# Kernel tuning notes

Hardware: AMD Instinct MI355X
Metric: run time of the kernel (lower is better)

Reference implementation:

```python
import jax, jax.numpy as jnp
import numpy as np

DATA_DIM = 2048
COORD_DIM = 2
NUM_V = DATA_DIM // COORD_DIM  # 1024 vertices
HID = 256
TDIM = 128
NUM_LAYERS = 4
B = 512


def _sinusoidal(t, dim=TDIM):
    half = dim // 2
    freqs = jnp.exp(-jnp.log(10000.0) * jnp.arange(half, dtype=jnp.float32) / (half - 1))
    ang = t.astype(jnp.float32)[:, None] * freqs[None, :]  # (B, half)
    return jnp.concatenate([jnp.sin(ang), jnp.cos(ang)], axis=1)  # (B, dim)


def _cycle_agg(h):
    # degree-3 cycle graph (self + next + prev), values 1/3 each == circular-shift mean
    # h: (B, V, D)
    return (h + jnp.roll(h, -1, axis=1) + jnp.roll(h, 1, axis=1)) * (1.0 / 3.0)


def setup_inputs() -> dict:
    key = jax.random.key(0)
    ks = jax.random.split(key, 16)
    dims = [COORD_DIM + TDIM] + [HID] * NUM_LAYERS  # [130,256,256,256,256]

    def glorot(k, shape):
        fan_in = shape[0]
        return jax.random.normal(k, shape, dtype=jnp.float32) / jnp.sqrt(jnp.float32(fan_in))

    inp = {
        'x': jax.random.normal(ks[0], (B, DATA_DIM), dtype=jnp.float32),
        't': jax.random.randint(ks[1], (B,), 0, 1000, dtype=jnp.int32),
        'time_W': glorot(ks[2], (TDIM, TDIM)),
        'time_b': jnp.zeros((TDIM,), jnp.float32),
        'W0': glorot(ks[3], (dims[0], dims[1])), 'b0': jnp.zeros((dims[1],), jnp.float32),
        'W1': glorot(ks[4], (dims[1], dims[2])), 'b1': jnp.zeros((dims[2],), jnp.float32),
        'W2': glorot(ks[5], (dims[2], dims[3])), 'b2': jnp.zeros((dims[3],), jnp.float32),
        'W3': glorot(ks[6], (dims[3], dims[4])), 'b3': jnp.zeros((dims[4],), jnp.float32),
        'res0_W': glorot(ks[7], (dims[0], dims[1])),
        'hW1': glorot(ks[8], (HID, HID)), 'hb1': jnp.zeros((HID,), jnp.float32),
        'hW2': glorot(ks[9], (HID, COORD_DIM)), 'hb2': jnp.zeros((COORD_DIM,), jnp.float32),
    }
    return inp


def reference(x, t, time_W, time_b, W0, b0, W1, b1, W2, b2, W3, b3, res0_W, hW1, hb1, hW2, hb2):
    silu = jax.nn.silu
    coords = x.reshape(B, NUM_V, COORD_DIM)
    temb = silu(_sinusoidal(t) @ time_W + time_b)  # (B, TDIM)
    temb = jnp.broadcast_to(temb[:, None, :], (B, NUM_V, TDIM))
    h = jnp.concatenate([coords, temb], axis=-1)  # (B, V, 130)

    Ws = [W0, W1, W2, W3]
    bs = [b0, b1, b2, b3]
    for i in range(NUM_LAYERS):
        residual = h @ res0_W if i == 0 else h
        # GraphConvolution: adj @ (h W) + b, with adj == normalized cycle aggregation
        h = _cycle_agg(h @ Ws[i]) + bs[i] + residual
        h = silu(h)

    h = silu(h @ hW1 + hb1) @ hW2 + hb2  # (B, V, 2)
    return h.reshape(B, DATA_DIM)
```

## Files before the change

### kernel.cpp

```cpp
#include <hip/hip_runtime.h>
#include <hip/hip_bf16.h>


typedef __attribute__((ext_vector_type(8))) short bf16x8;
typedef __attribute__((ext_vector_type(4))) float f32x4;

#define NV 1024

#define OFF_W0T   0
#define OFF_W1T   40960
#define OFF_W2T   106496
#define OFF_W3T   172032
#define OFF_HW1T  237568
#define OFF_HW2T  303104
#define OFF_TEMB  307200
#define PREP_ELEMS 307200

__device__ __forceinline__ float bf2f(short u){
  union { unsigned int i; float f; } v;
  v.i = ((unsigned int)(unsigned short)u) << 16;
  return v.f;
}
__device__ __forceinline__ short f2bf(float f){
  __hip_bfloat16 h = __float2bfloat16(f);
  return *reinterpret_cast<short*>(&h);
}
__device__ __forceinline__ float silu_f(float v){
  float e = __expf(-v);
  return v * __builtin_amdgcn_rcpf(1.f + e);
}
__device__ __forceinline__ f32x4 zero4(){ f32x4 z = {0.f,0.f,0.f,0.f}; return z; }
__device__ __forceinline__ unsigned int pack2_silu(float s0, float s1){
  return (unsigned int)(unsigned short)f2bf(silu_f(s0))
       | ((unsigned int)(unsigned short)f2bf(silu_f(s1)) << 16);
}

__global__ void prep_kernel(const float* __restrict__ W0, const float* __restrict__ res0,
                            const float* __restrict__ W1, const float* __restrict__ W2,
                            const float* __restrict__ W3, const float* __restrict__ hW1,
                            const float* __restrict__ hW2, short* __restrict__ ws){
  int idx = blockIdx.x * 256 + threadIdx.x;
  if (idx >= PREP_ELEMS) return;
  float v = 0.f;
  if (idx < 40960){
    int n = idx / 160, k = idx - n * 160;
    if (k < 128)      v = W0[(k + 2) * 256 + n] + res0[(k + 2) * 256 + n];
    else if (k < 130) v = W0[(k - 128) * 256 + n];
    else if (k < 132) v = res0[(k - 130) * 256 + n];
  } else if (idx < 303104){
    int rem = idx - 40960;
    int seg = rem >> 16;
    int r2 = rem & 65535;
    int n = r2 >> 8, k = r2 & 255;
    const float* src = (seg == 0) ? W1 : (seg == 1) ? W2 : (seg == 2) ? W3 : hW1;
    v = src[k * 256 + n];
    if (seg < 3) v *= (1.f / 3.f);
  } else {
    int rem = idx - 303104;
    int n = rem >> 8, k = rem & 255;
    if (n < 2) v = hW2[k * 2 + n];
  }
  ws[idx] = f2bf(v);
}

__global__ void temb_kernel(const int* __restrict__ t, const float* __restrict__ tW,
                            const float* __restrict__ tb, short* __restrict__ temb){
  __shared__ float sc[128];
  int b = blockIdx.x, n = threadIdx.x;
  float tv = (float)t[b];
  {
    int j = n & 63;
    float fr = __expf(-9.210340371976184f * (float)j * (1.f / 63.f));
    float ang = tv * fr;
    sc[n] = (n < 64) ? sinf(ang) : cosf(ang);
  }
  __syncthreads();
  float acc = tb[n];
  #pragma unroll 8
  for (int k = 0; k < 128; ++k) acc += sc[k] * tW[k * 128 + n];
  temb[b * 128 + n] = f2bf(silu_f(acc));
}

template<int KPAD>
__device__ __forceinline__ void mm2(const char* hbuf, const short* __restrict__ Wt,
                                    int m15, int g, int n0, f32x4 acc[5][2]){
  const short* wb = Wt + (n0 + 2 * m15) * KPAD + g * 8;
  #pragma unroll 4
  for (int ks = 0; ks < KPAD / 32; ++ks){
    bf16x8 bf0 = *(const bf16x8*)(wb + ks * 32);
    bf16x8 bf1 = *(const bf16x8*)(wb + KPAD + ks * 32);
    const int kb = ks * 64 + g * 16;
    #pragma unroll
    for (int mt = 0; mt < 5; ++mt){
      const int row = mt * 16 + m15;
      bf16x8 a = *(const bf16x8*)(hbuf + row * 512 + (kb ^ ((row & 7) << 4)));
      acc[mt][0] = __builtin_amdgcn_mfma_f32_16x16x32_bf16(a, bf0, acc[mt][0], 0, 0, 0);
      acc[mt][1] = __builtin_amdgcn_mfma_f32_16x16x32_bf16(a, bf1, acc[mt][1], 0, 0, 0);
    }
  }
}

__global__ __launch_bounds__(512, 4)
void gcn_fused(const float* __restrict__ x, const short* __restrict__ ws,
               const float* __restrict__ b0p, const float* __restrict__ b1p,
               const float* __restrict__ b2p, const float* __restrict__ b3p,
               const float* __restrict__ hb1p, const float* __restrict__ hb2p,
               float* __restrict__ out){
  extern __shared__ char lds[];
  char* const hA = lds;
  char* const hB = lds + 40960;
  const int tid = threadIdx.x;
  const int lane = tid & 63, wid = tid >> 6;
  const int m15 = lane & 15, g = lane >> 4;
  const int n0 = wid * 32;
  const int cb2 = (n0 + 2 * m15) * 2;
  const int b = blockIdx.y, v0 = blockIdx.x * 64;

  {
    const short* tembp = ws + OFF_TEMB + b * 128;
    for (int task = tid; task < 72 * 16; task += 512){
      int r = task >> 4, ck = (task & 15) * 16;
      *(bf16x8*)(hA + r * 512 + (ck ^ ((r & 7) << 4))) =
          *(const bf16x8*)(tembp + (task & 15) * 8);
    }
    for (int task = tid; task < 80 * 8; task += 512){
      int r = task >> 3, q = task & 7;
      bf16x8 v = {0, 0, 0, 0, 0, 0, 0, 0};
      if (q == 0 && r < 72){
        const float* xb = x + b * 2048;
        int vm = (v0 + r - 5) & (NV - 1);
        int vc = (v0 + r - 4) & (NV - 1);
        int vp = (v0 + r - 3) & (NV - 1);
        float c0m = xb[vm * 2], c1m = xb[vm * 2 + 1];
        float c0c = xb[vc * 2], c1c = xb[vc * 2 + 1];
        float c0p = xb[vp * 2], c1p = xb[vp * 2 + 1];
        v[0] = f2bf((c0m + c0c + c0p) * (1.f / 3.f));
        v[1] = f2bf((c1m + c1c + c1p) * (1.f / 3.f));
        v[2] = f2bf(c0c);
        v[3] = f2bf(c1c);
      }
      *(bf16x8*)(hA + r * 512 + (((16 + q) * 16) ^ ((r & 7) << 4))) = v;
    }
  }
  __syncthreads();

  f32x4 acc[5][2];

  {
    const float2 bias = *(const float2*)(b0p + n0 + 2 * m15);
    #pragma unroll
    for (int mt = 0; mt < 5; ++mt){ acc[mt][0] = zero4(); acc[mt][1] = zero4(); }
    mm2<160>(hA, ws + OFF_W0T, m15, g, n0, acc);
    #pragma unroll
    for (int mt = 0; mt < 5; ++mt){
      const int row0 = mt * 16 + g * 4;
      #pragma unroll
      for (int j = 0; j < 4; ++j){
        const int row = row0 + j;
        const int ad = row * 512 + (cb2 ^ ((row & 7) << 4));
        *(unsigned int*)(hB + ad) =
            pack2_silu(acc[mt][0][j] + bias.x, acc[mt][1][j] + bias.y);
      }
    }
  }
  __syncthreads();

  #pragma unroll
  for (int L = 0; L < 3; ++L){
    const char* bin  = (L & 1) ? hA : hB;
    char*       bout = (L & 1) ? hB : hA;
    const short* Wt = ws + (L == 0 ? OFF_W1T : L == 1 ? OFF_W2T : OFF_W3T);
    const float* bp = (L == 0 ? b1p : L == 1 ? b2p : b3p);
    const float2 bias = *(const float2*)(bp + n0 + 2 * m15);
    #pragma unroll
    for (int mt = 0; mt < 5; ++mt){ acc[mt][0] = zero4(); acc[mt][1] = zero4(); }
    mm2<256>(bin, Wt, m15, g, n0, acc);
    #pragma unroll
    for (int mt = 0; mt < 5; ++mt){
      float pm0[2], pp3[2];
      #pragma unroll
      for (int nt = 0; nt < 2; ++nt){
        float upv = (g == 3) ? acc[mt > 0 ? mt - 1 : 0][nt][3] : acc[mt][nt][3];
        pm0[nt] = __shfl(upv, (lane + 48) & 63);
        float dnv = (g == 0) ? acc[mt < 4 ? mt + 1 : 4][nt][0] : acc[mt][nt][0];
        pp3[nt] = __shfl(dnv, (lane + 16) & 63);
      }
      const int row0 = mt * 16 + g * 4;
      #pragma unroll
      for (int j = 0; j < 4; ++j){
        const int row = row0 + j;
        const int ad = row * 512 + (cb2 ^ ((row & 7) << 4));
        const unsigned int rr = *(const unsigned int*)(bin + ad);
        union { unsigned int i; float f; } re, ro;
        re.i = rr << 16;
        ro.i = rr & 0xffff0000u;
        float p0 = (j == 0) ? pm0[0] : acc[mt][0][j - 1];
        float n0v = (j == 3) ? pp3[0] : acc[mt][0][j + 1];
        float p1 = (j == 0) ? pm0[1] : acc[mt][1][j - 1];
        float n1v = (j == 3) ? pp3[1] : acc[mt][1][j + 1];
        float s0 = p0 + acc[mt][0][j] + n0v + bias.x + re.f;
        float s1 = p1 + acc[mt][1][j] + n1v + bias.y + ro.f;
        *(unsigned int*)(bout + ad) = pack2_silu(s0, s1);
      }
    }
    __syncthreads();
  }

  {
    const float2 bias = *(const float2*)(hb1p + n0 + 2 * m15);
    #pragma unroll
    for (int mt = 0; mt < 5; ++mt){ acc[mt][0] = zero4(); acc[mt][1] = zero4(); }
    mm2<256>(hA, ws + OFF_HW1T, m15, g, n0, acc);
    #pragma unroll
    for (int mt = 0; mt < 5; ++mt){
      const int row0 = mt * 16 + g * 4;
      #pragma unroll
      for (int j = 0; j < 4; ++j){
        const int row = row0 + j;
        const int ad = row * 512 + (cb2 ^ ((row & 7) << 4));
        *(unsigned int*)(hB + ad) =
            pack2_silu(acc[mt][0][j] + bias.x, acc[mt][1][j] + bias.y);
      }
    }
    __syncthreads();
  }

  if (wid < 5){
    f32x4 a2 = zero4();
    const short* wb = ws + OFF_HW2T + m15 * 256 + g * 8;
    const int row = wid * 16 + m15;
    const int rsw = row * 512;
    #pragma unroll 4
    for (int ks = 0; ks < 8; ++ks){
      bf16x8 bfr = *(const bf16x8*)(wb + ks * 32);
      const int kb = ks * 64 + g * 16;
      bf16x8 a = *(const bf16x8*)(hB + rsw + (kb ^ ((row & 7) << 4)));
      a2 = __builtin_amdgcn_mfma_f32_16x16x32_bf16(a, bfr, a2, 0, 0, 0);
    }
    if (m15 < 2){
      float bias = hb2p[m15];
      #pragma unroll
      for (int j = 0; j < 4; ++j){
        int orow = wid * 16 + g * 4 + j;
        if (orow >= 4 && orow < 68)
          out[b * 2048 + (v0 + orow - 4) * 2 + m15] = a2[j] + bias;
      }
    }
  }
}

extern "C" void kernel_launch(void* const* d_in, const int* in_sizes, int n_in,
                              void* d_out, int out_size, void* d_ws, size_t ws_size,
                              hipStream_t stream){
  const float* x   = (const float*)d_in[0];
  const int*   t   = (const int*)  d_in[1];
  const float* tW  = (const float*)d_in[2];
  const float* tb  = (const float*)d_in[3];
  const float* W0  = (const float*)d_in[4];
  const float* b0  = (const float*)d_in[5];
  const float* W1  = (const float*)d_in[6];
  const float* b1  = (const float*)d_in[7];
  const float* W2  = (const float*)d_in[8];
  const float* b2  = (const float*)d_in[9];
  const float* W3  = (const float*)d_in[10];
  const float* b3  = (const float*)d_in[11];
  const float* res0= (const float*)d_in[12];
  const float* hW1 = (const float*)d_in[13];
  const float* hb1 = (const float*)d_in[14];
  const float* hW2 = (const float*)d_in[15];
  const float* hb2 = (const float*)d_in[16];
  short* ws  = (short*)d_ws;
  float* out = (float*)d_out;

  hipFuncSetAttribute((const void*)gcn_fused,
                      hipFuncAttributeMaxDynamicSharedMemorySize, 81920);

  prep_kernel<<<dim3((PREP_ELEMS + 255) / 256), dim3(256), 0, stream>>>(
      W0, res0, W1, W2, W3, hW1, hW2, ws);
  temb_kernel<<<dim3(512), dim3(128), 0, stream>>>(t, tW, tb, ws + OFF_TEMB);
  gcn_fused<<<dim3(16, 512), dim3(512), 81920, stream>>>(
      x, ws, b0, b1, b2, b3, hb1, hb2, out);
}
```

Measured before the change: 777.6 us.

## Factor layer-0 time-embedding projection out per batch and drop the layer-0 MFMA

Layer 0's input is a per-batch time embedding plus two coordinates per vertex, so the time part of (W0+res0) is computed once per batch row in temb_kernel. The fused kernel then builds layer-0 activations with a 4-term FMA on per-vertex coordinates instead of a K=160 MFMA GEMM over every vertex tile. This removes the redundant per-tile layer-0 matmul and the staging of the time embedding into LDS. In exchange it adds a small fp32 GEMV per batch row and changes the ping-pong buffer order. It also adds s_setprio around the MFMA loops.

```diff
diff --git a/kernel.cpp b/kernel.cpp
--- a/kernel.cpp
+++ b/kernel.cpp
@@ -7,23 +7,24 @@
 
 #define NV 1024
 
-#define OFF_W0T   0
-#define OFF_W1T   40960
-#define OFF_W2T   106496
-#define OFF_W3T   172032
-#define OFF_HW1T  237568
-#define OFF_HW2T  303104
-#define OFF_TEMB  307200
-#define PREP_ELEMS 307200
-
+#define OFF_W1T   0
+#define OFF_W2T   65536
+#define OFF_W3T   131072
+#define OFF_HW1T  196608
+#define OFF_HW2T  262144
+#define BF16_ELEMS 266240
+#define CW_BYTE   532480
+#define TV_BYTE   536576
+#define PREP_TOTAL (BF16_ELEMS + 1024)
+
+__device__ __forceinline__ short f2bf(float f){
+  __hip_bfloat16 h = __float2bfloat16(f);
+  return *reinterpret_cast<short*>(&h);
+}
 __device__ __forceinline__ float bf2f(short u){
   union { unsigned int i; float f; } v;
   v.i = ((unsigned int)(unsigned short)u) << 16;
   return v.f;
-}
-__device__ __forceinline__ short f2bf(float f){
-  __hip_bfloat16 h = __float2bfloat16(f);
-  return *reinterpret_cast<short*>(&h);
 }
 __device__ __forceinline__ float silu_f(float v){
   float e = __expf(-v);
@@ -40,55 +41,67 @@
                             const float* __restrict__ W3, const float* __restrict__ hW1,
                             const float* __restrict__ hW2, short* __restrict__ ws){
   int idx = blockIdx.x * 256 + threadIdx.x;
-  if (idx >= PREP_ELEMS) return;
-  float v = 0.f;
-  if (idx < 40960){
-    int n = idx / 160, k = idx - n * 160;
-    if (k < 128)      v = W0[(k + 2) * 256 + n] + res0[(k + 2) * 256 + n];
-    else if (k < 130) v = W0[(k - 128) * 256 + n];
-    else if (k < 132) v = res0[(k - 130) * 256 + n];
-  } else if (idx < 303104){
-    int rem = idx - 40960;
-    int seg = rem >> 16;
-    int r2 = rem & 65535;
-    int n = r2 >> 8, k = r2 & 255;
-    const float* src = (seg == 0) ? W1 : (seg == 1) ? W2 : (seg == 2) ? W3 : hW1;
-    v = src[k * 256 + n];
-    if (seg < 3) v *= (1.f / 3.f);
+  if (idx >= PREP_TOTAL) return;
+  if (idx < BF16_ELEMS){
+    float v;
+    if (idx < 262144){
+      int seg = idx >> 16;
+      int r2 = idx & 65535;
+      int n = r2 >> 8, k = r2 & 255;
+      const float* src = (seg == 0) ? W1 : (seg == 1) ? W2 : (seg == 2) ? W3 : hW1;
+      v = src[k * 256 + n];
+      if (seg < 3) v *= (1.f / 3.f);
+    } else {
+      int rem = idx - 262144;
+      int n = rem >> 8, k = rem & 255;
+      v = (n < 2) ? hW2[k * 2 + n] : 0.f;
+    }
+    ws[idx] = f2bf(v);
   } else {
-    int rem = idx - 303104;
-    int n = rem >> 8, k = rem & 255;
-    if (n < 2) v = hW2[k * 2 + n];
-  }
-  ws[idx] = f2bf(v);
+    int i = idx - BF16_ELEMS;
+    int d = i >> 8, n = i & 255;
+    float v = (d < 2) ? W0[d * 256 + n] : res0[(d - 2) * 256 + n];
+    ((float*)((char*)ws + CW_BYTE))[i] = v;
+  }
 }
 
 __global__ void temb_kernel(const int* __restrict__ t, const float* __restrict__ tW,
-                            const float* __restrict__ tb, short* __restrict__ temb){
+                            const float* __restrict__ tb, const float* __restrict__ W0,
+                            const float* __restrict__ res0, const float* __restrict__ b0,
+                            float* __restrict__ tv){
   __shared__ float sc[128];
+  __shared__ float tmb[128];
   int b = blockIdx.x, n = threadIdx.x;
-  float tv = (float)t[b];
-  {
+  float tvt = (float)t[b];
+  if (n < 128){
     int j = n & 63;
     float fr = __expf(-9.210340371976184f * (float)j * (1.f / 63.f));
-    float ang = tv * fr;
+    float ang = tvt * fr;
     sc[n] = (n < 64) ? sinf(ang) : cosf(ang);
   }
   __syncthreads();
-  float acc = tb[n];
-  #pragma unroll 8
-  for (int k = 0; k < 128; ++k) acc += sc[k] * tW[k * 128 + n];
-  temb[b * 128 + n] = f2bf(silu_f(acc));
-}
-
-template<int KPAD>
-__device__ __forceinline__ void mm2(const char* hbuf, const short* __restrict__ Wt,
-                                    int m15, int g, int n0, f32x4 acc[5][2]){
-  const short* wb = Wt + (n0 + 2 * m15) * KPAD + g * 8;
+  if (n < 128){
+    float acc = tb[n];
+    #pragma unroll 8
+    for (int k = 0; k < 128; ++k) acc += sc[k] * tW[k * 128 + n];
+    tmb[n] = silu_f(acc);
+  }
+  __syncthreads();
+  float acc2 = b0[n];
   #pragma unroll 4
-  for (int ks = 0; ks < KPAD / 32; ++ks){
+  for (int k = 0; k < 128; ++k)
+    acc2 += tmb[k] * (W0[(k + 2) * 256 + n] + res0[(k + 2) * 256 + n]);
+  tv[b * 256 + n] = acc2;
+}
+
+__device__ __forceinline__ void mm2_256(const char* hbuf, const short* __restrict__ Wt,
+                                        int m15, int g, int n0, f32x4 acc[5][2]){
+  const short* wb = Wt + (n0 + 2 * m15) * 256 + g * 8;
+  __builtin_amdgcn_s_setprio(1);
+  #pragma unroll 4
+  for (int ks = 0; ks < 8; ++ks){
     bf16x8 bf0 = *(const bf16x8*)(wb + ks * 32);
-    bf16x8 bf1 = *(const bf16x8*)(wb + KPAD + ks * 32);
+    bf16x8 bf1 = *(const bf16x8*)(wb + 256 + ks * 32);
     const int kb = ks * 64 + g * 16;
     #pragma unroll
     for (int mt = 0; mt < 5; ++mt){
@@ -98,14 +111,15 @@
       acc[mt][1] = __builtin_amdgcn_mfma_f32_16x16x32_bf16(a, bf1, acc[mt][1], 0, 0, 0);
     }
   }
+  __builtin_amdgcn_s_setprio(0);
 }
 
 __global__ __launch_bounds__(512, 4)
 void gcn_fused(const float* __restrict__ x, const short* __restrict__ ws,
-               const float* __restrict__ b0p, const float* __restrict__ b1p,
-               const float* __restrict__ b2p, const float* __restrict__ b3p,
-               const float* __restrict__ hb1p, const float* __restrict__ hb2p,
-               float* __restrict__ out){
+               const float* __restrict__ tvp, const float* __restrict__ cwf,
+               const float* __restrict__ b1p, const float* __restrict__ b2p,
+               const float* __restrict__ b3p, const float* __restrict__ hb1p,
+               const float* __restrict__ hb2p, float* __restrict__ out){
   extern __shared__ char lds[];
   char* const hA = lds;
   char* const hB = lds + 40960;
@@ -113,68 +127,62 @@
   const int lane = tid & 63, wid = tid >> 6;
   const int m15 = lane & 15, g = lane >> 4;
   const int n0 = wid * 32;
-  const int cb2 = (n0 + 2 * m15) * 2;
+  const int col0 = n0 + 2 * m15;
+  const int cb2 = col0 * 2;
   const int b = blockIdx.y, v0 = blockIdx.x * 64;
 
+  if (tid < 80){
+    const int r = tid;
+    const float* xb = x + b * 2048;
+    int vm = (v0 + r - 5) & (NV - 1);
+    int vc = (v0 + r - 4) & (NV - 1);
+    int vp = (v0 + r - 3) & (NV - 1);
+    float c0m = xb[vm * 2], c1m = xb[vm * 2 + 1];
+    float c0c = xb[vc * 2], c1c = xb[vc * 2 + 1];
+    float c0p = xb[vp * 2], c1p = xb[vp * 2 + 1];
+    f32x4 cc;
+    cc[0] = (c0m + c0c + c0p) * (1.f / 3.f);
+    cc[1] = (c1m + c1c + c1p) * (1.f / 3.f);
+    cc[2] = c0c;
+    cc[3] = c1c;
+    *(f32x4*)(hB + r * 16) = cc;
+  }
+  __syncthreads();
+
   {
-    const short* tembp = ws + OFF_TEMB + b * 128;
-    for (int task = tid; task < 72 * 16; task += 512){
-      int r = task >> 4, ck = (task & 15) * 16;
-      *(bf16x8*)(hA + r * 512 + (ck ^ ((r & 7) << 4))) =
-          *(const bf16x8*)(tembp + (task & 15) * 8);
-    }
-    for (int task = tid; task < 80 * 8; task += 512){
-      int r = task >> 3, q = task & 7;
-      bf16x8 v = {0, 0, 0, 0, 0, 0, 0, 0};
-      if (q == 0 && r < 72){
-        const float* xb = x + b * 2048;
-        int vm = (v0 + r - 5) & (NV - 1);
-        int vc = (v0 + r - 4) & (NV - 1);
-        int vp = (v0 + r - 3) & (NV - 1);
-        float c0m = xb[vm * 2], c1m = xb[vm * 2 + 1];
-        float c0c = xb[vc * 2], c1c = xb[vc * 2 + 1];
-        float c0p = xb[vp * 2], c1p = xb[vp * 2 + 1];
-        v[0] = f2bf((c0m + c0c + c0p) * (1.f / 3.f));
-        v[1] = f2bf((c1m + c1c + c1p) * (1.f / 3.f));
-        v[2] = f2bf(c0c);
-        v[3] = f2bf(c1c);
-      }
-      *(bf16x8*)(hA + r * 512 + (((16 + q) * 16) ^ ((r & 7) << 4))) = v;
+    const float2 tv2 = *(const float2*)(tvp + b * 256 + col0);
+    const float2 wA = *(const float2*)(cwf + col0);
+    const float2 wB = *(const float2*)(cwf + 256 + col0);
+    const float2 wC = *(const float2*)(cwf + 512 + col0);
+    const float2 wD = *(const float2*)(cwf + 768 + col0);
+    #pragma unroll
+    for (int mt = 0; mt < 5; ++mt){
+      const int row0 = mt * 16 + g * 4;
+      #pragma unroll
+      for (int j = 0; j < 4; ++j){
+        const int row = row0 + j;
+        const f32x4 cc = *(const f32x4*)(hB + row * 16);
+        float s0 = tv2.x + cc[0] * wA.x + cc[1] * wB.x + cc[2] * wC.x + cc[3] * wD.x;
+        float s1 = tv2.y + cc[0] * wA.y + cc[1] * wB.y + cc[2] * wC.y + cc[3] * wD.y;
+        const int ad = row * 512 + (cb2 ^ ((row & 7) << 4));
+        *(unsigned int*)(hA + ad) = pack2_silu(s0, s1);
+      }
     }
   }
   __syncthreads();
 
   f32x4 acc[5][2];
-
-  {
-    const float2 bias = *(const float2*)(b0p + n0 + 2 * m15);
-    #pragma unroll
-    for (int mt = 0; mt < 5; ++mt){ acc[mt][0] = zero4(); acc[mt][1] = zero4(); }
-    mm2<160>(hA, ws + OFF_W0T, m15, g, n0, acc);
-    #pragma unroll
-    for (int mt = 0; mt < 5; ++mt){
-      const int row0 = mt * 16 + g * 4;
-      #pragma unroll
-      for (int j = 0; j < 4; ++j){
-        const int row = row0 + j;
-        const int ad = row * 512 + (cb2 ^ ((row & 7) << 4));
-        *(unsigned int*)(hB + ad) =
-            pack2_silu(acc[mt][0][j] + bias.x, acc[mt][1][j] + bias.y);
-      }
-    }
-  }
-  __syncthreads();
 
   #pragma unroll
   for (int L = 0; L < 3; ++L){
-    const char* bin  = (L & 1) ? hA : hB;
-    char*       bout = (L & 1) ? hB : hA;
+    const char* bin  = (L & 1) ? hB : hA;
+    char*       bout = (L & 1) ? hA : hB;
     const short* Wt = ws + (L == 0 ? OFF_W1T : L == 1 ? OFF_W2T : OFF_W3T);
     const float* bp = (L == 0 ? b1p : L == 1 ? b2p : b3p);
-    const float2 bias = *(const float2*)(bp + n0 + 2 * m15);
+    const float2 bias = *(const float2*)(bp + col0);
     #pragma unroll
     for (int mt = 0; mt < 5; ++mt){ acc[mt][0] = zero4(); acc[mt][1] = zero4(); }
-    mm2<256>(bin, Wt, m15, g, n0, acc);
+    mm2_256(bin, Wt, m15, g, n0, acc);
     #pragma unroll
     for (int mt = 0; mt < 5; ++mt){
       float pm0[2], pp3[2];
@@ -207,10 +215,10 @@
   }
 
   {
-    const float2 bias = *(const float2*)(hb1p + n0 + 2 * m15);
+    const float2 bias = *(const float2*)(hb1p + col0);
     #pragma unroll
     for (int mt = 0; mt < 5; ++mt){ acc[mt][0] = zero4(); acc[mt][1] = zero4(); }
-    mm2<256>(hA, ws + OFF_HW1T, m15, g, n0, acc);
+    mm2_256(hB, ws + OFF_HW1T, m15, g, n0, acc);
     #pragma unroll
     for (int mt = 0; mt < 5; ++mt){
       const int row0 = mt * 16 + g * 4;
@@ -218,7 +226,7 @@
       for (int j = 0; j < 4; ++j){
         const int row = row0 + j;
         const int ad = row * 512 + (cb2 ^ ((row & 7) << 4));
-        *(unsigned int*)(hB + ad) =
+        *(unsigned int*)(hA + ad) =
             pack2_silu(acc[mt][0][j] + bias.x, acc[mt][1][j] + bias.y);
       }
     }
@@ -234,7 +242,7 @@
     for (int ks = 0; ks < 8; ++ks){
       bf16x8 bfr = *(const bf16x8*)(wb + ks * 32);
       const int kb = ks * 64 + g * 16;
-      bf16x8 a = *(const bf16x8*)(hB + rsw + (kb ^ ((row & 7) << 4)));
+      bf16x8 a = *(const bf16x8*)(hA + rsw + (kb ^ ((row & 7) << 4)));
       a2 = __builtin_amdgcn_mfma_f32_16x16x32_bf16(a, bfr, a2, 0, 0, 0);
     }
     if (m15 < 2){
@@ -270,14 +278,16 @@
   const float* hW2 = (const float*)d_in[15];
   const float* hb2 = (const float*)d_in[16];
   short* ws  = (short*)d_ws;
+  float* tvp = (float*)((char*)d_ws + TV_BYTE);
+  float* cwf = (float*)((char*)d_ws + CW_BYTE);
   float* out = (float*)d_out;
 
   hipFuncSetAttribute((const void*)gcn_fused,
                       hipFuncAttributeMaxDynamicSharedMemorySize, 81920);
 
-  prep_kernel<<<dim3((PREP_ELEMS + 255) / 256), dim3(256), 0, stream>>>(
+  prep_kernel<<<dim3((PREP_TOTAL + 255) / 256), dim3(256), 0, stream>>>(
       W0, res0, W1, W2, W3, hW1, hW2, ws);
-  temb_kernel<<<dim3(512), dim3(128), 0, stream>>>(t, tW, tb, ws + OFF_TEMB);
+  temb_kernel<<<dim3(512), dim3(256), 0, stream>>>(t, tW, tb, W0, res0, b0, tvp);
   gcn_fused<<<dim3(16, 512), dim3(512), 81920, stream>>>(
-      x, ws, b0, b1, b2, b3, hb1, hb2, out);
-}
+      x, ws, tvp, cwf, b1, b2, b3, hb1, hb2, out);
+}
```

After: 712.0 us. -8.4%, faster.
